# Kernel tuning notes

Measured on AMD Instinct MI355X. Metric: run time of the kernel, lower is better.

Reference implementation:

```python
import jax, jax.numpy as jnp
import numpy as np

C = 512
GROUPS = 16
EPS = 1e-6


def group_norm(x, gamma, beta):
    # x: (b, c, h, w)
    b, c, h, w = x.shape
    xg = x.reshape(b, GROUPS, c // GROUPS, h, w)
    mean = xg.mean(axis=(2, 3, 4), keepdims=True)
    var = xg.var(axis=(2, 3, 4), keepdims=True)
    xn = ((xg - mean) * jax.lax.rsqrt(var + EPS)).reshape(b, c, h, w)
    return xn * gamma[None, :, None, None] + beta[None, :, None, None]


def setup_inputs() -> dict:
    key = jax.random.key(0)
    ks = jax.random.split(key, 9)
    scale = 1.0 / np.sqrt(C)
    x = jax.random.normal(ks[0], (32, C, 32, 32), dtype=jnp.float32)
    return {
        "x": x,
        "gn_gamma": jnp.ones((C,), jnp.float32),
        "gn_beta": jnp.zeros((C,), jnp.float32),
        "wq": jax.random.normal(ks[1], (C, C), jnp.float32) * scale,
        "bq": jnp.zeros((C,), jnp.float32),
        "wk": jax.random.normal(ks[2], (C, C), jnp.float32) * scale,
        "bk": jnp.zeros((C,), jnp.float32),
        "wv": jax.random.normal(ks[3], (C, C), jnp.float32) * scale,
        "bv": jnp.zeros((C,), jnp.float32),
        "wp": jax.random.normal(ks[4], (C, C), jnp.float32) * scale,
        "bp": jnp.zeros((C,), jnp.float32),
    }


def reference(x, gn_gamma, gn_beta, wq, bq, wk, bk, wv, bv, wp, bp):
    b, c, h, w = x.shape
    hn = group_norm(x, gn_gamma, gn_beta).reshape(b, c, h * w)  # (b, c, n)
    # 1x1 convs == per-token channel GEMMs
    q = jnp.einsum('oc,bcn->bon', wq, hn) + bq[None, :, None]
    k = jnp.einsum('oc,bcn->bon', wk, hn) + bk[None, :, None]
    v = jnp.einsum('oc,bcn->bon', wv, hn) + bv[None, :, None]
    # scores: (b, n, m) = q^T k, scaled
    s = jnp.einsum('bcn,bcm->bnm', q, k) * (float(c) ** -0.5)
    # original subtracts the global max (shift-invariant) then softmax over dim 2
    s = s - jnp.max(s)
    attn = jax.nn.softmax(s, axis=2)
    # h_ = v @ attn^T  -> (b, c, n)
    out = jnp.einsum('bcm,bnm->bcn', v, attn)
    out = jnp.einsum('oc,bcn->bon', wp, out) + bp[None, :, None]
    return x + out.reshape(b, c, h, w)
```

## Files before the change

### kernel.cpp

```cpp
#include <hip/hip_runtime.h>
#include <hip/hip_bf16.h>

typedef unsigned short u16;
typedef __attribute__((ext_vector_type(8))) short bf16x8;
typedef __attribute__((ext_vector_type(4))) float f32x4;

#define BK 32
#define TILE_ELEMS (128 * BK)

__device__ __forceinline__ u16 f2bf(float f) {
  union { float f; unsigned u; } a; a.f = f;
  unsigned r = a.u + 0x7fffu + ((a.u >> 16) & 1u);
  return (u16)(r >> 16);
}

__device__ __forceinline__ u16 f2h(float f) {
  union { _Float16 h; u16 u; } c; c.h = (_Float16)f; return c.u;
}

__device__ __forceinline__ void stage_async(const u16* __restrict__ g, int ldg,
                                            u16* __restrict__ s, int tid) {
  int lane = tid & 63, wave = tid >> 6;
#pragma unroll
  for (int t = 0; t < 2; ++t) {
    int chunk = (wave * 2 + t) * 64 + lane;
    int row = chunk >> 2, koff = (chunk & 3) << 3;
    __builtin_amdgcn_global_load_lds(
        (const __attribute__((address_space(1))) unsigned int*)(g + (long)row * ldg + koff),
        (__attribute__((address_space(3))) unsigned int*)(s + (wave * 2 + t) * 512),
        16, 0, 0);
  }
}

__device__ __forceinline__ void gemm_core(
    const u16* __restrict__ Ab, const u16* __restrict__ Bb,
    int lda, int ldb, int K, int tid,
    u16* __restrict__ As, u16* __restrict__ Bs, f32x4 (&acc)[4][4]) {
  int wave = tid >> 6, lane = tid & 63;
  int wr = wave >> 1, wc = wave & 1;
  int lrow = lane & 15, quad = lane >> 4;
#pragma unroll
  for (int i = 0; i < 4; ++i)
#pragma unroll
    for (int j = 0; j < 4; ++j) acc[i][j] = (f32x4){0.f, 0.f, 0.f, 0.f};
  stage_async(Ab, lda, As, tid);
  stage_async(Bb, ldb, Bs, tid);
  int cur = 0;
  for (int k0 = 0; k0 < K; k0 += BK) {
    __syncthreads();
    if (k0 + BK < K) {
      stage_async(Ab + k0 + BK, lda, As + (cur ^ 1) * TILE_ELEMS, tid);
      stage_async(Bb + k0 + BK, ldb, Bs + (cur ^ 1) * TILE_ELEMS, tid);
    }
    const u16* Ac = As + cur * TILE_ELEMS;
    const u16* Bc = Bs + cur * TILE_ELEMS;
    bf16x8 af[4], bfr[4];
#pragma unroll
    for (int mt = 0; mt < 4; ++mt)
      af[mt] = *(const bf16x8*)&Ac[(wr * 64 + mt * 16 + lrow) * BK + quad * 8];
#pragma unroll
    for (int nt = 0; nt < 4; ++nt)
      bfr[nt] = *(const bf16x8*)&Bc[(wc * 64 + nt * 16 + lrow) * BK + quad * 8];
#pragma unroll
    for (int mt = 0; mt < 4; ++mt)
#pragma unroll
      for (int nt = 0; nt < 4; ++nt)
        acc[mt][nt] = __builtin_amdgcn_mfma_f32_16x16x32_bf16(af[mt], bfr[nt], acc[mt][nt], 0, 0, 0);
    cur ^= 1;
  }
}

__device__ __forceinline__ void epi_trans_bf16(
    f32x4 (&acc)[4][4], u16* __restrict__ C, long cbase, int m0, int n0, int ldc,
    const float* __restrict__ bias, float scale, int tid) {
  int wave = tid >> 6, lane = tid & 63;
  int wr = wave >> 1, wc = wave & 1;
  int lrow = lane & 15, quad = lane >> 4;
#pragma unroll
  for (int mt = 0; mt < 4; ++mt) {
    int rowbase = m0 + wr * 64 + mt * 16 + quad * 4;
    float4 b4 = bias ? *(const float4*)&bias[rowbase] : make_float4(0.f, 0.f, 0.f, 0.f);
#pragma unroll
    for (int nt = 0; nt < 4; ++nt) {
      int col = n0 + wc * 64 + nt * 16 + lrow;
      f32x4 a = acc[mt][nt];
      uint2 o;
      o.x = (unsigned)f2bf(a[0] * scale + b4.x) | ((unsigned)f2bf(a[1] * scale + b4.y) << 16);
      o.y = (unsigned)f2bf(a[2] * scale + b4.z) | ((unsigned)f2bf(a[3] * scale + b4.w) << 16);
      *(uint2*)(C + cbase + (long)col * ldc + rowbase) = o;
    }
  }
}

template <int MODE>
__global__ __launch_bounds__(256) void gemm_kernel(
    const u16* __restrict__ Ag, const u16* __restrict__ Bg,
    void* __restrict__ C0, void* __restrict__ C1, void* __restrict__ C2,
    const float* __restrict__ bias0, const float* __restrict__ bias1,
    const float* __restrict__ bias2, const float* __restrict__ resid,
    int lda, int ldb, int ldc,
    long strideA, long strideB, long strideC, int K, float scale) {
  __shared__ u16 As[2 * TILE_ELEMS];
  __shared__ u16 Bs[2 * TILE_ELEMS];
  int tid = threadIdx.x;
  int b = blockIdx.z;
  int m0 = blockIdx.y * 128, n0 = blockIdx.x * 128;
  const u16* Ab = Ag + (long)b * strideA + (long)m0 * lda;
  const u16* Bb = Bg + (long)b * strideB + (long)n0 * ldb;
  f32x4 acc[4][4];
  gemm_core(Ab, Bb, lda, ldb, K, tid, As, Bs, acc);

  int wave = tid >> 6, lane = tid & 63;
  int wr = wave >> 1, wc = wave & 1;
  int lrow = lane & 15, quad = lane >> 4;
  long cbase = (long)b * strideC;

  if (MODE == 0) {
    epi_trans_bf16(acc, (u16*)C0, cbase, m0, n0, ldc, bias0, scale, tid);
  } else if (MODE == 1) {
#pragma unroll
    for (int mt = 0; mt < 4; ++mt)
#pragma unroll
      for (int r = 0; r < 4; ++r) {
        int row = m0 + wr * 64 + mt * 16 + quad * 4 + r;
#pragma unroll
        for (int nt = 0; nt < 4; ++nt) {
          int col = n0 + wc * 64 + nt * 16 + lrow;
          ((u16*)C0)[cbase + (long)row * ldc + col] = f2h(acc[mt][nt][r] * scale);
        }
      }
  } else if (MODE == 2) {
#pragma unroll
    for (int mt = 0; mt < 4; ++mt)
#pragma unroll
      for (int r = 0; r < 4; ++r) {
        int row = m0 + wr * 64 + mt * 16 + quad * 4 + r;
        float bv = bias0[row];
#pragma unroll
        for (int nt = 0; nt < 4; ++nt) {
          int col = n0 + wc * 64 + nt * 16 + lrow;
          long idx = cbase + (long)row * ldc + col;
          ((float*)C0)[idx] = acc[mt][nt][r] * scale + bv + resid[idx];
        }
      }
  } else {
    int seg = m0 >> 9;
    int ml = m0 & 511;
    if (seg == 0) {
      epi_trans_bf16(acc, (u16*)C0, cbase, ml, n0, 512, bias0, 1.f, tid);
    } else if (seg == 1) {
      epi_trans_bf16(acc, (u16*)C1, cbase, ml, n0, 512, bias1, 1.f, tid);
    } else {
#pragma unroll
      for (int mt = 0; mt < 4; ++mt)
#pragma unroll
        for (int r = 0; r < 4; ++r) {
          int row = ml + wr * 64 + mt * 16 + quad * 4 + r;
          float bv = bias2[row];
#pragma unroll
          for (int nt = 0; nt < 4; ++nt) {
            int col = n0 + wc * 64 + nt * 16 + lrow;
            ((u16*)C2)[cbase + (long)row * 1024 + col] = f2bf(acc[mt][nt][r] + bv);
          }
        }
    }
  }
}

__global__ __launch_bounds__(256) void groupnorm_kernel(
    const float* __restrict__ x, const float* __restrict__ gamma,
    const float* __restrict__ beta, u16* __restrict__ hnT) {
  int g = blockIdx.x, b = blockIdx.y;
  const float* xb = x + ((long)b * 512 + g * 32) * 1024;
  int tid = threadIdx.x;
  float s = 0.f, sq = 0.f;
  float4 vals[32];
#pragma unroll
  for (int j = 0; j < 32; ++j) {
    float4 v = *(const float4*)(xb + (long)j * 1024 + tid * 4);
    vals[j] = v;
    s += v.x + v.y + v.z + v.w;
    sq += v.x * v.x + v.y * v.y + v.z * v.z + v.w * v.w;
  }
#pragma unroll
  for (int off = 1; off < 64; off <<= 1) {
    s += __shfl_xor(s, off);
    sq += __shfl_xor(sq, off);
  }
  __shared__ float ls[4], lq[4];
  if ((tid & 63) == 0) { ls[tid >> 6] = s; lq[tid >> 6] = sq; }
  __syncthreads();
  float ts = ls[0] + ls[1] + ls[2] + ls[3];
  float tq = lq[0] + lq[1] + lq[2] + lq[3];
  float mean = ts * (1.f / 32768.f);
  float var = tq * (1.f / 32768.f) - mean * mean;
  float rstd = rsqrtf(var + 1e-6f);
  u16* hb = hnT + (long)b * (1024 * 512) + g * 32;
#pragma unroll
  for (int t = 0; t < 4; ++t) {
    u16 row[32];
#pragma unroll
    for (int j = 0; j < 32; ++j) {
      float xv = ((const float*)&vals[j])[t];
      row[j] = f2bf((xv - mean) * rstd * gamma[g * 32 + j] + beta[g * 32 + j]);
    }
    uint4* dst = (uint4*)(hb + (long)(tid * 4 + t) * 512);
    const uint4* src = (const uint4*)row;
    dst[0] = src[0]; dst[1] = src[1]; dst[2] = src[2]; dst[3] = src[3];
  }
}

__global__ __launch_bounds__(256) void softmax_kernel(u16* __restrict__ s) {
  long row = blockIdx.x;
  u16* sr = s + row * 1024;
  int tid = threadIdx.x;
  union { uint2 u; _Float16 h[4]; } c;
  c.u = *(const uint2*)(sr + tid * 4);
  float v0 = (float)c.h[0], v1 = (float)c.h[1], v2 = (float)c.h[2], v3 = (float)c.h[3];
  float m = fmaxf(fmaxf(v0, v1), fmaxf(v2, v3));
#pragma unroll
  for (int off = 1; off < 64; off <<= 1) m = fmaxf(m, __shfl_xor(m, off));
  __shared__ float lm[4], lsum[4];
  if ((tid & 63) == 0) lm[tid >> 6] = m;
  __syncthreads();
  float rowmax = fmaxf(fmaxf(lm[0], lm[1]), fmaxf(lm[2], lm[3]));
  float e0 = expf(v0 - rowmax), e1 = expf(v1 - rowmax);
  float e2 = expf(v2 - rowmax), e3 = expf(v3 - rowmax);
  float sum = e0 + e1 + e2 + e3;
#pragma unroll
  for (int off = 1; off < 64; off <<= 1) sum += __shfl_xor(sum, off);
  if ((tid & 63) == 0) lsum[tid >> 6] = sum;
  __syncthreads();
  float inv = 1.f / (lsum[0] + lsum[1] + lsum[2] + lsum[3]);
  uint2 o;
  o.x = (unsigned)f2bf(e0 * inv) | ((unsigned)f2bf(e1 * inv) << 16);
  o.y = (unsigned)f2bf(e2 * inv) | ((unsigned)f2bf(e3 * inv) << 16);
  *(uint2*)(sr + tid * 4) = o;
}

__global__ __launch_bounds__(256) void convertw_kernel(
    const float* __restrict__ w0, const float* __restrict__ w1,
    const float* __restrict__ w2, const float* __restrict__ w3,
    u16* __restrict__ out) {
  int wsel = blockIdx.x >> 8;
  const float* src = wsel == 0 ? w0 : wsel == 1 ? w1 : wsel == 2 ? w2 : w3;
  int idx = ((blockIdx.x & 255) * 256 + threadIdx.x) * 4;
  float4 v = *(const float4*)(src + idx);
  uint2 o;
  o.x = (unsigned)f2bf(v.x) | ((unsigned)f2bf(v.y) << 16);
  o.y = (unsigned)f2bf(v.z) | ((unsigned)f2bf(v.w) << 16);
  *(uint2*)(out + (long)wsel * 262144 + idx) = o;
}

extern "C" void kernel_launch(void* const* d_in, const int* in_sizes, int n_in,
                              void* d_out, int out_size, void* d_ws, size_t ws_size,
                              hipStream_t stream) {
  const float* x     = (const float*)d_in[0];
  const float* gamma = (const float*)d_in[1];
  const float* beta  = (const float*)d_in[2];
  const float* wq    = (const float*)d_in[3];
  const float* bq    = (const float*)d_in[4];
  const float* wk    = (const float*)d_in[5];
  const float* bk    = (const float*)d_in[6];
  const float* wv    = (const float*)d_in[7];
  const float* bv    = (const float*)d_in[8];
  const float* wp    = (const float*)d_in[9];
  const float* bp    = (const float*)d_in[10];
  float* out = (float*)d_out;
  char* ws = (char*)d_ws;

  u16* wbf = (u16*)ws;
  u16* hnT = (u16*)(ws + (2L << 20));
  u16* qT  = (u16*)(ws + (34L << 20));
  u16* kT  = (u16*)(ws + (66L << 20));
  u16* v   = (u16*)(ws + (98L << 20));
  u16* s16 = (u16*)(ws + (130L << 20));
  u16* aoT = hnT;

  const long SB = 512L * 1024;
  const long SS = 1024L * 1024;
  const float scale = 0.044194173824159216f;

  convertw_kernel<<<1024, 256, 0, stream>>>(wq, wk, wv, wp, wbf);
  groupnorm_kernel<<<dim3(16, 32), 256, 0, stream>>>(x, gamma, beta, hnT);

  gemm_kernel<3><<<dim3(8, 12, 32), 256, 0, stream>>>(
      wbf, hnT, qT, kT, v, bq, bk, bv, nullptr,
      512, 512, 0, 0, SB, SB, 512, 1.f);

  gemm_kernel<1><<<dim3(8, 8, 32), 256, 0, stream>>>(
      qT, kT, s16, nullptr, nullptr, nullptr, nullptr, nullptr, nullptr,
      512, 512, 1024, SB, SB, SS, 512, scale);

  softmax_kernel<<<32 * 1024, 256, 0, stream>>>(s16);

  gemm_kernel<0><<<dim3(8, 4, 32), 256, 0, stream>>>(
      v, s16, aoT, nullptr, nullptr, nullptr, nullptr, nullptr, nullptr,
      1024, 1024, 512, SB, SS, SB, 1024, 1.f);

  gemm_kernel<2><<<dim3(8, 4, 32), 256, 0, stream>>>(
      wbf + 3 * 262144, aoT, out, nullptr, nullptr, bp, nullptr, nullptr, x,
      512, 512, 1024, 0, SB, SB, 512, 1.f);
}
```

Measured before the change: 426.8 us.

## Triple-buffer GEMM LDS staging with vmcnt waits and XOR-swizzled K chunks

Moves the GEMM main loop from double to triple buffering. It prefetches two K tiles ahead and waits with explicit s_waitcnt vmcnt counts before the barrier, instead of a plain __syncthreads. It also XOR-swizzles the 16-byte K chunk position by row when loading into LDS and reading fragments, to cut LDS bank conflicts. The cost is 50% more LDS per block, which may lower occupancy, and reliance on hand-counted vmcnt values matching the four async loads issued per stage.

```diff
diff --git a/kernel.cpp b/kernel.cpp
--- a/kernel.cpp
+++ b/kernel.cpp
@@ -7,6 +7,7 @@
 
 #define BK 32
 #define TILE_ELEMS (128 * BK)
+#define NBUF 3
 
 __device__ __forceinline__ u16 f2bf(float f) {
   union { float f; unsigned u; } a; a.f = f;
@@ -24,9 +25,10 @@
 #pragma unroll
   for (int t = 0; t < 2; ++t) {
     int chunk = (wave * 2 + t) * 64 + lane;
-    int row = chunk >> 2, koff = (chunk & 3) << 3;
+    int row = chunk >> 2;
+    int q = (chunk & 3) ^ ((row >> 1) & 3);
     __builtin_amdgcn_global_load_lds(
-        (const __attribute__((address_space(1))) unsigned int*)(g + (long)row * ldg + koff),
+        (const __attribute__((address_space(1))) unsigned int*)(g + (long)row * ldg + (q << 3)),
         (__attribute__((address_space(3))) unsigned int*)(s + (wave * 2 + t) * 512),
         16, 0, 0);
   }
@@ -39,34 +41,43 @@
   int wave = tid >> 6, lane = tid & 63;
   int wr = wave >> 1, wc = wave & 1;
   int lrow = lane & 15, quad = lane >> 4;
+  int koff = ((quad ^ ((lrow >> 1) & 3)) << 3);
 #pragma unroll
   for (int i = 0; i < 4; ++i)
 #pragma unroll
     for (int j = 0; j < 4; ++j) acc[i][j] = (f32x4){0.f, 0.f, 0.f, 0.f};
+  int ntiles = K / BK;
   stage_async(Ab, lda, As, tid);
   stage_async(Bb, ldb, Bs, tid);
+  if (ntiles > 1) {
+    stage_async(Ab + BK, lda, As + TILE_ELEMS, tid);
+    stage_async(Bb + BK, ldb, Bs + TILE_ELEMS, tid);
+  }
   int cur = 0;
-  for (int k0 = 0; k0 < K; k0 += BK) {
-    __syncthreads();
-    if (k0 + BK < K) {
-      stage_async(Ab + k0 + BK, lda, As + (cur ^ 1) * TILE_ELEMS, tid);
-      stage_async(Bb + k0 + BK, ldb, Bs + (cur ^ 1) * TILE_ELEMS, tid);
+  for (int t = 0; t < ntiles; ++t) {
+    if (t + 1 < ntiles) asm volatile("s_waitcnt vmcnt(4)" ::: "memory");
+    else                asm volatile("s_waitcnt vmcnt(0)" ::: "memory");
+    __builtin_amdgcn_s_barrier();
+    if (t + 2 < ntiles) {
+      int nxt = cur + 2; if (nxt >= NBUF) nxt -= NBUF;
+      stage_async(Ab + (t + 2) * BK, lda, As + nxt * TILE_ELEMS, tid);
+      stage_async(Bb + (t + 2) * BK, ldb, Bs + nxt * TILE_ELEMS, tid);
     }
     const u16* Ac = As + cur * TILE_ELEMS;
     const u16* Bc = Bs + cur * TILE_ELEMS;
     bf16x8 af[4], bfr[4];
 #pragma unroll
     for (int mt = 0; mt < 4; ++mt)
-      af[mt] = *(const bf16x8*)&Ac[(wr * 64 + mt * 16 + lrow) * BK + quad * 8];
-#pragma unroll
-    for (int nt = 0; nt < 4; ++nt)
-      bfr[nt] = *(const bf16x8*)&Bc[(wc * 64 + nt * 16 + lrow) * BK + quad * 8];
+      af[mt] = *(const bf16x8*)&Ac[(wr * 64 + mt * 16 + lrow) * BK + koff];
+#pragma unroll
+    for (int nb = 0; nb < 4; ++nb)
+      bfr[nb] = *(const bf16x8*)&Bc[(wc * 64 + nb * 16 + lrow) * BK + koff];
 #pragma unroll
     for (int mt = 0; mt < 4; ++mt)
 #pragma unroll
-      for (int nt = 0; nt < 4; ++nt)
-        acc[mt][nt] = __builtin_amdgcn_mfma_f32_16x16x32_bf16(af[mt], bfr[nt], acc[mt][nt], 0, 0, 0);
-    cur ^= 1;
+      for (int nb = 0; nb < 4; ++nb)
+        acc[mt][nb] = __builtin_amdgcn_mfma_f32_16x16x32_bf16(af[mt], bfr[nb], acc[mt][nb], 0, 0, 0);
+    ++cur; if (cur == NBUF) cur = 0;
   }
 }
 
@@ -100,8 +111,8 @@
     const float* __restrict__ bias2, const float* __restrict__ resid,
     int lda, int ldb, int ldc,
     long strideA, long strideB, long strideC, int K, float scale) {
-  __shared__ u16 As[2 * TILE_ELEMS];
-  __shared__ u16 Bs[2 * TILE_ELEMS];
+  __shared__ u16 As[NBUF * TILE_ELEMS];
+  __shared__ u16 Bs[NBUF * TILE_ELEMS];
   int tid = threadIdx.x;
   int b = blockIdx.z;
   int m0 = blockIdx.y * 128, n0 = blockIdx.x * 128;
```

Measured after the change: 426.9 us. Within noise of the previous version (+0.0%).

## Switch GEMMs to 256x256 tiles with 8 waves and interleaved LDS pipeline

Applied to the files above, without the earlier changes.

Replaces the 128x128, 4-wave double-buffered GEMM core with a 256x256 tile computed by 8 waves. Each K=64 step is split into four 128-row half-tiles, and async global->LDS loads are interleaved between MFMA quadrants using explicit barriers, vmcnt/lgkmcnt waits and s_setprio. LDS rows are XOR-swizzled to avoid bank conflicts, and 128KB of dynamic shared memory is requested. The goal is more data reuse per tile and better overlap of loads with MFMA work, at the cost of fewer blocks per grid, many barriers and a tighter register budget.

```diff
diff --git a/kernel.cpp b/kernel.cpp
--- a/kernel.cpp
+++ b/kernel.cpp
@@ -5,8 +5,9 @@
 typedef __attribute__((ext_vector_type(8))) short bf16x8;
 typedef __attribute__((ext_vector_type(4))) float f32x4;
 
-#define BK 32
-#define TILE_ELEMS (128 * BK)
+#define FENCE asm volatile("" ::: "memory")
+#define BARRIER() do { FENCE; __builtin_amdgcn_s_barrier(); FENCE; } while (0)
+#define LGKM0 asm volatile("s_waitcnt lgkmcnt(0)" ::: "memory")
 
 __device__ __forceinline__ u16 f2bf(float f) {
   union { float f; unsigned u; } a; a.f = f;
@@ -18,72 +19,143 @@
   union { _Float16 h; u16 u; } c; c.h = (_Float16)f; return c.u;
 }
 
-__device__ __forceinline__ void stage_async(const u16* __restrict__ g, int ldg,
-                                            u16* __restrict__ s, int tid) {
+__device__ __forceinline__ void stage_ht(const u16* __restrict__ g, int ldg,
+                                         u16* __restrict__ s, int tid) {
   int lane = tid & 63, wave = tid >> 6;
 #pragma unroll
   for (int t = 0; t < 2; ++t) {
-    int chunk = (wave * 2 + t) * 64 + lane;
-    int row = chunk >> 2, koff = (chunk & 3) << 3;
+    int cbase = t * 512 + wave * 64;
+    int c = cbase + lane;
+    int row = c >> 3;
+    int q = (c & 7) ^ (((row >> 2) & 3) << 1);
     __builtin_amdgcn_global_load_lds(
-        (const __attribute__((address_space(1))) unsigned int*)(g + (long)row * ldg + koff),
-        (__attribute__((address_space(3))) unsigned int*)(s + (wave * 2 + t) * 512),
+        (const __attribute__((address_space(1))) unsigned int*)(g + (long)row * ldg + (q << 3)),
+        (__attribute__((address_space(3))) unsigned int*)(s + cbase * 8),
         16, 0, 0);
   }
 }
 
-__device__ __forceinline__ void gemm_core(
+__device__ __forceinline__ void ld_a(const u16* __restrict__ Ah, int mh,
+                                     int lrow, int quad, int sw, bf16x8 (&a)[4][2]) {
+#pragma unroll
+  for (int i = 0; i < 4; ++i) {
+    int rb = (mh * 64 + i * 16 + lrow) * 64;
+#pragma unroll
+    for (int ks = 0; ks < 2; ++ks)
+      a[i][ks] = *(const bf16x8*)&Ah[rb + (((ks * 4 + quad) ^ sw) << 3)];
+  }
+}
+
+__device__ __forceinline__ void ld_b(const u16* __restrict__ Bh, int wn1, int nh,
+                                     int lrow, int quad, int sw, bf16x8 (&bq)[2][2]) {
+#pragma unroll
+  for (int j = 0; j < 2; ++j) {
+    int rb = (wn1 * 64 + (nh * 2 + j) * 16 + lrow) * 64;
+#pragma unroll
+    for (int ks = 0; ks < 2; ++ks)
+      bq[j][ks] = *(const bf16x8*)&Bh[rb + (((ks * 4 + quad) ^ sw) << 3)];
+  }
+}
+
+template <int MH, int NH>
+__device__ __forceinline__ void mfma_q(bf16x8 (&a)[4][2], bf16x8 (&bq)[2][2],
+                                       f32x4 (&acc)[8][4]) {
+#pragma unroll
+  for (int i = 0; i < 4; ++i)
+#pragma unroll
+    for (int j = 0; j < 2; ++j) {
+      f32x4 c = acc[MH * 4 + i][NH * 2 + j];
+      c = __builtin_amdgcn_mfma_f32_16x16x32_bf16(a[i][0], bq[j][0], c, 0, 0, 0);
+      c = __builtin_amdgcn_mfma_f32_16x16x32_bf16(a[i][1], bq[j][1], c, 0, 0, 0);
+      acc[MH * 4 + i][NH * 2 + j] = c;
+    }
+}
+
+__device__ __forceinline__ void gemm256_core(
     const u16* __restrict__ Ab, const u16* __restrict__ Bb,
     int lda, int ldb, int K, int tid,
-    u16* __restrict__ As, u16* __restrict__ Bs, f32x4 (&acc)[4][4]) {
+    u16* __restrict__ As, u16* __restrict__ Bs, f32x4 (&acc)[8][4]) {
   int wave = tid >> 6, lane = tid & 63;
-  int wr = wave >> 1, wc = wave & 1;
+  int wm = wave >> 2, wn = wave & 3, wn1 = wn & 1;
   int lrow = lane & 15, quad = lane >> 4;
-#pragma unroll
-  for (int i = 0; i < 4; ++i)
+  int sw = ((lrow >> 2) & 3) << 1;
+#pragma unroll
+  for (int i = 0; i < 8; ++i)
 #pragma unroll
     for (int j = 0; j < 4; ++j) acc[i][j] = (f32x4){0.f, 0.f, 0.f, 0.f};
-  stage_async(Ab, lda, As, tid);
-  stage_async(Bb, ldb, Bs, tid);
-  int cur = 0;
-  for (int k0 = 0; k0 < K; k0 += BK) {
-    __syncthreads();
-    if (k0 + BK < K) {
-      stage_async(Ab + k0 + BK, lda, As + (cur ^ 1) * TILE_ELEMS, tid);
-      stage_async(Bb + k0 + BK, ldb, Bs + (cur ^ 1) * TILE_ELEMS, tid);
-    }
-    const u16* Ac = As + cur * TILE_ELEMS;
-    const u16* Bc = Bs + cur * TILE_ELEMS;
-    bf16x8 af[4], bfr[4];
-#pragma unroll
-    for (int mt = 0; mt < 4; ++mt)
-      af[mt] = *(const bf16x8*)&Ac[(wr * 64 + mt * 16 + lrow) * BK + quad * 8];
-#pragma unroll
-    for (int nt = 0; nt < 4; ++nt)
-      bfr[nt] = *(const bf16x8*)&Bc[(wc * 64 + nt * 16 + lrow) * BK + quad * 8];
-#pragma unroll
-    for (int mt = 0; mt < 4; ++mt)
-#pragma unroll
-      for (int nt = 0; nt < 4; ++nt)
-        acc[mt][nt] = __builtin_amdgcn_mfma_f32_16x16x32_bf16(af[mt], bfr[nt], acc[mt][nt], 0, 0, 0);
-    cur ^= 1;
+  const u16* Ah0 = As + wm * 8192;
+  const u16* Ah1 = As + (2 + wm) * 8192;
+  const u16* Bh0 = Bs + (wn >> 1) * 8192;
+  const u16* Bh1 = Bs + (2 + (wn >> 1)) * 8192;
+  int nkt = K >> 6, npair = nkt >> 1;
+  stage_ht(Ab, lda, As, tid);
+  stage_ht(Ab + 128L * lda, lda, As + 8192, tid);
+  stage_ht(Bb, ldb, Bs, tid);
+  stage_ht(Bb + 128L * ldb, ldb, Bs + 8192, tid);
+  stage_ht(Ab + 64, lda, As + 2 * 8192, tid);
+  bf16x8 a[4][2], bq0[2][2], bq1[2][2];
+  for (int pr = 0; pr < npair; ++pr) {
+    int kt1 = pr * 2 + 1, kt2 = kt1 + 1, kt3 = kt1 + 2;
+    bool st2 = kt2 < nkt, st3 = kt3 < nkt;
+    asm volatile("s_waitcnt vmcnt(2)" ::: "memory");
+    BARRIER();
+    ld_a(Ah0, 0, lrow, quad, sw, a);
+    ld_b(Bh0, wn1, 0, lrow, quad, sw, bq0);
+    stage_ht(Ab + 128L * lda + kt1 * 64, lda, As + 3 * 8192, tid);
+    BARRIER(); LGKM0;
+    __builtin_amdgcn_s_setprio(1); mfma_q<0, 0>(a, bq0, acc); __builtin_amdgcn_s_setprio(0);
+    BARRIER();
+    ld_b(Bh0, wn1, 1, lrow, quad, sw, bq1);
+    stage_ht(Bb + kt1 * 64, ldb, Bs + 2 * 8192, tid);
+    BARRIER(); LGKM0;
+    __builtin_amdgcn_s_setprio(1); mfma_q<0, 1>(a, bq1, acc); __builtin_amdgcn_s_setprio(0);
+    BARRIER();
+    ld_a(Ah0, 1, lrow, quad, sw, a);
+    stage_ht(Bb + 128L * ldb + kt1 * 64, ldb, Bs + 3 * 8192, tid);
+    BARRIER(); LGKM0;
+    __builtin_amdgcn_s_setprio(1); mfma_q<1, 1>(a, bq1, acc); __builtin_amdgcn_s_setprio(0);
+    BARRIER();
+    if (st2) stage_ht(Ab + kt2 * 64, lda, As, tid);
+    BARRIER(); LGKM0;
+    __builtin_amdgcn_s_setprio(1); mfma_q<1, 0>(a, bq0, acc); __builtin_amdgcn_s_setprio(0);
+    BARRIER();
+    if (pr + 1 < npair) asm volatile("s_waitcnt vmcnt(2)" ::: "memory");
+    else                asm volatile("s_waitcnt vmcnt(0)" ::: "memory");
+    BARRIER();
+    ld_a(Ah1, 0, lrow, quad, sw, a);
+    ld_b(Bh1, wn1, 0, lrow, quad, sw, bq0);
+    if (st2) stage_ht(Ab + 128L * lda + kt2 * 64, lda, As + 8192, tid);
+    BARRIER(); LGKM0;
+    __builtin_amdgcn_s_setprio(1); mfma_q<0, 0>(a, bq0, acc); __builtin_amdgcn_s_setprio(0);
+    BARRIER();
+    ld_b(Bh1, wn1, 1, lrow, quad, sw, bq1);
+    if (st2) stage_ht(Bb + kt2 * 64, ldb, Bs, tid);
+    BARRIER(); LGKM0;
+    __builtin_amdgcn_s_setprio(1); mfma_q<0, 1>(a, bq1, acc); __builtin_amdgcn_s_setprio(0);
+    BARRIER();
+    ld_a(Ah1, 1, lrow, quad, sw, a);
+    if (st2) stage_ht(Bb + 128L * ldb + kt2 * 64, ldb, Bs + 8192, tid);
+    BARRIER(); LGKM0;
+    __builtin_amdgcn_s_setprio(1); mfma_q<1, 1>(a, bq1, acc); __builtin_amdgcn_s_setprio(0);
+    BARRIER();
+    if (st3) stage_ht(Ab + kt3 * 64, lda, As + 2 * 8192, tid);
+    BARRIER(); LGKM0;
+    __builtin_amdgcn_s_setprio(1); mfma_q<1, 0>(a, bq0, acc); __builtin_amdgcn_s_setprio(0);
+    BARRIER();
   }
 }
 
 __device__ __forceinline__ void epi_trans_bf16(
-    f32x4 (&acc)[4][4], u16* __restrict__ C, long cbase, int m0, int n0, int ldc,
-    const float* __restrict__ bias, float scale, int tid) {
-  int wave = tid >> 6, lane = tid & 63;
-  int wr = wave >> 1, wc = wave & 1;
-  int lrow = lane & 15, quad = lane >> 4;
-#pragma unroll
-  for (int mt = 0; mt < 4; ++mt) {
-    int rowbase = m0 + wr * 64 + mt * 16 + quad * 4;
+    f32x4 (&acc)[8][4], u16* __restrict__ C, long cbase, int m0, int n0, int ldc,
+    const float* __restrict__ bias, float scale, int wm, int wn, int lrow, int quad) {
+#pragma unroll
+  for (int mf = 0; mf < 8; ++mf) {
+    int rowbase = m0 + wm * 128 + mf * 16 + quad * 4;
     float4 b4 = bias ? *(const float4*)&bias[rowbase] : make_float4(0.f, 0.f, 0.f, 0.f);
 #pragma unroll
-    for (int nt = 0; nt < 4; ++nt) {
-      int col = n0 + wc * 64 + nt * 16 + lrow;
-      f32x4 a = acc[mt][nt];
+    for (int nf = 0; nf < 4; ++nf) {
+      int col = n0 + wn * 64 + nf * 16 + lrow;
+      f32x4 a = acc[mf][nf];
       uint2 o;
       o.x = (unsigned)f2bf(a[0] * scale + b4.x) | ((unsigned)f2bf(a[1] * scale + b4.y) << 16);
       o.y = (unsigned)f2bf(a[2] * scale + b4.z) | ((unsigned)f2bf(a[3] * scale + b4.w) << 16);
@@ -93,74 +165,75 @@
 }
 
 template <int MODE>
-__global__ __launch_bounds__(256) void gemm_kernel(
+__global__ __launch_bounds__(512, 2) void gemm_kernel(
     const u16* __restrict__ Ag, const u16* __restrict__ Bg,
     void* __restrict__ C0, void* __restrict__ C1, void* __restrict__ C2,
     const float* __restrict__ bias0, const float* __restrict__ bias1,
     const float* __restrict__ bias2, const float* __restrict__ resid,
     int lda, int ldb, int ldc,
     long strideA, long strideB, long strideC, int K, float scale) {
-  __shared__ u16 As[2 * TILE_ELEMS];
-  __shared__ u16 Bs[2 * TILE_ELEMS];
+  extern __shared__ u16 smem[];
+  u16* As = smem;
+  u16* Bs = smem + 32768;
   int tid = threadIdx.x;
   int b = blockIdx.z;
-  int m0 = blockIdx.y * 128, n0 = blockIdx.x * 128;
+  int m0 = blockIdx.y * 256, n0 = blockIdx.x * 256;
   const u16* Ab = Ag + (long)b * strideA + (long)m0 * lda;
   const u16* Bb = Bg + (long)b * strideB + (long)n0 * ldb;
-  f32x4 acc[4][4];
-  gemm_core(Ab, Bb, lda, ldb, K, tid, As, Bs, acc);
+  f32x4 acc[8][4];
+  gemm256_core(Ab, Bb, lda, ldb, K, tid, As, Bs, acc);
 
   int wave = tid >> 6, lane = tid & 63;
-  int wr = wave >> 1, wc = wave & 1;
+  int wm = wave >> 2, wn = wave & 3;
   int lrow = lane & 15, quad = lane >> 4;
   long cbase = (long)b * strideC;
 
   if (MODE == 0) {
-    epi_trans_bf16(acc, (u16*)C0, cbase, m0, n0, ldc, bias0, scale, tid);
+    epi_trans_bf16(acc, (u16*)C0, cbase, m0, n0, ldc, bias0, scale, wm, wn, lrow, quad);
   } else if (MODE == 1) {
 #pragma unroll
-    for (int mt = 0; mt < 4; ++mt)
+    for (int mf = 0; mf < 8; ++mf)
 #pragma unroll
       for (int r = 0; r < 4; ++r) {
-        int row = m0 + wr * 64 + mt * 16 + quad * 4 + r;
-#pragma unroll
-        for (int nt = 0; nt < 4; ++nt) {
-          int col = n0 + wc * 64 + nt * 16 + lrow;
-          ((u16*)C0)[cbase + (long)row * ldc + col] = f2h(acc[mt][nt][r] * scale);
+        int row = m0 + wm * 128 + mf * 16 + quad * 4 + r;
+#pragma unroll
+        for (int nf = 0; nf < 4; ++nf) {
+          int col = n0 + wn * 64 + nf * 16 + lrow;
+          ((u16*)C0)[cbase + (long)row * ldc + col] = f2h(acc[mf][nf][r] * scale);
         }
       }
   } else if (MODE == 2) {
 #pragma unroll
-    for (int mt = 0; mt < 4; ++mt)
+    for (int mf = 0; mf < 8; ++mf)
 #pragma unroll
       for (int r = 0; r < 4; ++r) {
-        int row = m0 + wr * 64 + mt * 16 + quad * 4 + r;
+        int row = m0 + wm * 128 + mf * 16 + quad * 4 + r;
         float bv = bias0[row];
 #pragma unroll
-        for (int nt = 0; nt < 4; ++nt) {
-          int col = n0 + wc * 64 + nt * 16 + lrow;
+        for (int nf = 0; nf < 4; ++nf) {
+          int col = n0 + wn * 64 + nf * 16 + lrow;
           long idx = cbase + (long)row * ldc + col;
-          ((float*)C0)[idx] = acc[mt][nt][r] * scale + bv + resid[idx];
+          ((float*)C0)[idx] = acc[mf][nf][r] * scale + bv + resid[idx];
         }
       }
   } else {
     int seg = m0 >> 9;
     int ml = m0 & 511;
     if (seg == 0) {
-      epi_trans_bf16(acc, (u16*)C0, cbase, ml, n0, 512, bias0, 1.f, tid);
+      epi_trans_bf16(acc, (u16*)C0, cbase, ml, n0, 512, bias0, 1.f, wm, wn, lrow, quad);
     } else if (seg == 1) {
-      epi_trans_bf16(acc, (u16*)C1, cbase, ml, n0, 512, bias1, 1.f, tid);
+      epi_trans_bf16(acc, (u16*)C1, cbase, ml, n0, 512, bias1, 1.f, wm, wn, lrow, quad);
     } else {
 #pragma unroll
-      for (int mt = 0; mt < 4; ++mt)
+      for (int mf = 0; mf < 8; ++mf)
 #pragma unroll
         for (int r = 0; r < 4; ++r) {
-          int row = ml + wr * 64 + mt * 16 + quad * 4 + r;
+          int row = ml + wm * 128 + mf * 16 + quad * 4 + r;
           float bv = bias2[row];
 #pragma unroll
-          for (int nt = 0; nt < 4; ++nt) {
-            int col = n0 + wc * 64 + nt * 16 + lrow;
-            ((u16*)C2)[cbase + (long)row * 1024 + col] = f2bf(acc[mt][nt][r] + bv);
+          for (int nf = 0; nf < 4; ++nf) {
+            int col = n0 + wn * 64 + nf * 16 + lrow;
+            ((u16*)C2)[cbase + (long)row * 1024 + col] = f2bf(acc[mf][nf][r] + bv);
           }
         }
     }
@@ -269,6 +342,15 @@
   float* out = (float*)d_out;
   char* ws = (char*)d_ws;
 
+  static int attr_done = 0;
+  if (!attr_done) {
+    hipFuncSetAttribute((const void*)gemm_kernel<0>, hipFuncAttributeMaxDynamicSharedMemorySize, 131072);
+    hipFuncSetAttribute((const void*)gemm_kernel<1>, hipFuncAttributeMaxDynamicSharedMemorySize, 131072);
+    hipFuncSetAttribute((const void*)gemm_kernel<2>, hipFuncAttributeMaxDynamicSharedMemorySize, 131072);
+    hipFuncSetAttribute((const void*)gemm_kernel<3>, hipFuncAttributeMaxDynamicSharedMemorySize, 131072);
+    attr_done = 1;
+  }
+
   u16* wbf = (u16*)ws;
   u16* hnT = (u16*)(ws + (2L << 20));
   u16* qT  = (u16*)(ws + (34L << 20));
@@ -284,21 +366,21 @@
   convertw_kernel<<<1024, 256, 0, stream>>>(wq, wk, wv, wp, wbf);
   groupnorm_kernel<<<dim3(16, 32), 256, 0, stream>>>(x, gamma, beta, hnT);
 
-  gemm_kernel<3><<<dim3(8, 12, 32), 256, 0, stream>>>(
+  gemm_kernel<3><<<dim3(4, 6, 32), 512, 131072, stream>>>(
       wbf, hnT, qT, kT, v, bq, bk, bv, nullptr,
       512, 512, 0, 0, SB, SB, 512, 1.f);
 
-  gemm_kernel<1><<<dim3(8, 8, 32), 256, 0, stream>>>(
+  gemm_kernel<1><<<dim3(4, 4, 32), 512, 131072, stream>>>(
       qT, kT, s16, nullptr, nullptr, nullptr, nullptr, nullptr, nullptr,
       512, 512, 1024, SB, SB, SS, 512, scale);
 
   softmax_kernel<<<32 * 1024, 256, 0, stream>>>(s16);
 
-  gemm_kernel<0><<<dim3(8, 4, 32), 256, 0, stream>>>(
+  gemm_kernel<0><<<dim3(4, 2, 32), 512, 131072, stream>>>(
       v, s16, aoT, nullptr, nullptr, nullptr, nullptr, nullptr, nullptr,
       1024, 1024, 512, SB, SS, SB, 1024, 1.f);
 
-  gemm_kernel<2><<<dim3(8, 4, 32), 256, 0, stream>>>(
+  gemm_kernel<2><<<dim3(4, 2, 32), 512, 131072, stream>>>(
       wbf + 3 * 262144, aoT, out, nullptr, nullptr, bp, nullptr, nullptr, x,
       512, 512, 1024, 0, SB, SB, 512, 1.f);
 }
```

Result: faster. 377.9 us (-11.5%).
